# Optimization experiments

Measured on AMD Instinct MI355X. Metric: run time of the kernel, lower is better.

## Reference

```python
import jax, jax.numpy as jnp
import numpy as np

K = 20          # neighbors
EPS = 1e-5      # batch-norm eps (torch default)


def setup_inputs() -> dict:
    key = jax.random.key(0)
    k1, k2 = jax.random.split(key, 2)
    B, C, N = 16, 3, 2048
    out_dims, in_dims = 64, 2 * C
    x = jax.random.normal(k1, (B, C, N), dtype=jnp.float32)
    # Conv2d 1x1 weight, kaiming-style init as in init_layer: std = sqrt(2/(1*1*out))
    W = jax.random.normal(k2, (out_dims, in_dims), dtype=jnp.float32) * np.float32(np.sqrt(2.0 / out_dims))
    bn_weight = jnp.ones((out_dims,), dtype=jnp.float32)
    bn_bias = jnp.zeros((out_dims,), dtype=jnp.float32)
    return {"x": x, "W": W, "bn_weight": bn_weight, "bn_bias": bn_bias}


def _get_graph_feature(x, k):
    # x: (B, C, N)
    xx = jnp.sum(x * x, axis=1)                       # (B, N) squared norms
    inner = jnp.einsum('bcn,bcm->bnm', x, x)          # (B, N, N)
    pd = -xx[:, :, None] + 2.0 * inner - xx[:, None, :]  # -||xi - xj||^2
    _, idx = jax.lax.top_k(pd, k)                     # (B, N, k) nearest neighbors
    xt = jnp.transpose(x, (0, 2, 1))                  # (B, N, C)
    # gather neighbor features per batch: (N, C)[ (N, k) ] -> (N, k, C)
    neigh = jax.vmap(lambda feats, ind: feats[ind])(xt, idx)   # (B, N, k, C)
    center = jnp.broadcast_to(xt[:, :, None, :], neigh.shape)  # (B, N, k, C)
    feat = jnp.concatenate([neigh - center, center], axis=-1)  # (B, N, k, 2C)
    return jnp.transpose(feat, (0, 3, 1, 2))          # (B, 2C, N, k)


def reference(x, W, bn_weight, bn_bias):
    feat = _get_graph_feature(x, K)                   # (B, 2C, N, k)
    y = jnp.einsum('oc,bcnk->bonk', W, feat)          # 1x1 conv, no bias
    # BatchNorm2d_fw: fresh running stats + training=True -> plain batch stats
    mean = jnp.mean(y, axis=(0, 2, 3), keepdims=True)
    var = jnp.var(y, axis=(0, 2, 3), keepdims=True)   # biased variance
    yn = (y - mean) * jax.lax.rsqrt(var + EPS)
    yn = yn * bn_weight[None, :, None, None] + bn_bias[None, :, None, None]
    out = jnp.max(jax.nn.relu(yn), axis=-1)           # max over k -> (B, 64, N)
    return out
```

## Files before the change

### kernel.cpp

```cpp
#include <hip/hip_runtime.h>
#include <math.h>

#define B_   16
#define N_   2048
#define KNN  20
#define OD   64
#define M_TOT (B_ * N_ * KNN)
#define PPB  64
#define NB   64
#define CAP  96
#define BKT_BASE 468

typedef unsigned long long u64;
typedef unsigned int u32;
typedef unsigned short u16;

__global__ __launch_bounds__(512, 4) void k1_knn(const float* __restrict__ x,
                                                 float* __restrict__ stats,
                                                 int* __restrict__ idxbuf) {
    __shared__ float4 pts[N_];
    __shared__ u32    hist[NB * PPB];
    __shared__ u16    coll[PPB][CAP];
    __shared__ u32    pcnt[PPB];
    __shared__ u32    edgev[PPB];

    const int b     = blockIdx.x >> 5;
    const int chunk = blockIdx.x & 31;
    const int t     = threadIdx.x;

    const float* xb = x + b * 3 * N_;
    for (int n = t; n < N_; n += 512) {
        float x0 = xb[n], x1 = xb[N_ + n], x2 = xb[2 * N_ + n];
        float xx = x0 * x0;
        xx = fmaf(x1, x1, xx);
        xx = fmaf(x2, x2, xx);
        pts[n] = make_float4(x0, x1, x2, xx);
    }
    for (int i = t; i < NB * PPB; i += 512) hist[i] = 0;
    if (t < PPB) pcnt[t] = 0;
    __syncthreads();

    const int p  = t & 63;
    const int s  = t >> 6;
    const int il = chunk * 64 + p;
    const float4 pi = pts[il];
    const int j0 = s << 8;

    for (int jj = 0; jj < 256; jj += 8) {
        float4 q[8];
#pragma unroll
        for (int u = 0; u < 8; ++u) q[u] = pts[j0 + jj + u];
#pragma unroll
        for (int u = 0; u < 8; ++u) {
            float dot = pi.x * q[u].x;
            dot = fmaf(pi.y, q[u].y, dot);
            dot = fmaf(pi.z, q[u].z, dot);
            float pd = fmaf(2.f, dot, -pi.w) - q[u].w;
            u32 nk = __float_as_uint(pd) & 0x7FFFFFFFu;
            int bkt = (int)(nk >> 21) - BKT_BASE;
            bkt = min(max(bkt, 0), 63);
            atomicAdd(&hist[bkt * PPB + p], 1u);
        }
    }
    __syncthreads();

    if (t < PPB) {
        int cum = 0, tau = 63;
        for (int k = 0; k < NB; ++k) {
            cum += (int)hist[k * PPB + t];
            if (cum >= KNN) { tau = k; break; }
        }
        edgev[t] = (u32)(BKT_BASE + 1 + tau) << 21;
    }
    __syncthreads();

    {
        const u32 edge = edgev[p];
        for (int jj = 0; jj < 256; jj += 8) {
            float4 q[8];
#pragma unroll
            for (int u = 0; u < 8; ++u) q[u] = pts[j0 + jj + u];
#pragma unroll
            for (int u = 0; u < 8; ++u) {
                float dot = pi.x * q[u].x;
                dot = fmaf(pi.y, q[u].y, dot);
                dot = fmaf(pi.z, q[u].z, dot);
                float pd = fmaf(2.f, dot, -pi.w) - q[u].w;
                u32 nk = __float_as_uint(pd) & 0x7FFFFFFFu;
                if (nk < edge) {
                    u32 pos = atomicAdd(&pcnt[p], 1u);
                    if (pos < CAP) coll[p][pos] = (u16)(j0 + jj + u);
                }
            }
        }
    }
    __syncthreads();

    if (t < PPB) {
        const int cnt = min((int)pcnt[t], CAP);
        u64 d[KNN];
#pragma unroll
        for (int q = 0; q < KNN; ++q) d[q] = 0ull;
        for (int e = 0; e < cnt; ++e) {
            int j = coll[t][e];
            float4 pj = pts[j];
            float dot = pi.x * pj.x;
            dot = fmaf(pi.y, pj.y, dot);
            dot = fmaf(pi.z, pj.z, dot);
            float pd = fmaf(2.f, dot, -pi.w) - pj.w;
            u32 u = __float_as_uint(pd);
            u32 mono = ((int)u < 0) ? ~u : (u | 0x80000000u);
            u64 v = ((u64)mono << 32) | (u32)(~j);
            if (v > d[KNN - 1]) {
#pragma unroll
                for (int q = 0; q < KNN; ++q) {
                    u64 hi = (v > d[q]) ? v : d[q];
                    u64 lo = (v > d[q]) ? d[q] : v;
                    d[q] = hi; v = lo;
                }
            }
        }
        int ri[KNN];
#pragma unroll
        for (int r = 0; r < KNN; ++r) ri[r] = ~(u32)d[r];

        int* op = idxbuf + (b * N_ + il) * KNN;
#pragma unroll
        for (int r = 0; r < KNN; ++r) op[r] = ri[r];

        float se0 = 0.f, se1 = 0.f, se2 = 0.f;
        float see[6] = {0.f, 0.f, 0.f, 0.f, 0.f, 0.f};
#pragma unroll
        for (int r = 0; r < KNN; ++r) {
            float4 pj = pts[ri[r]];
            float e0 = pj.x - pi.x, e1 = pj.y - pi.y, e2 = pj.z - pi.z;
            se0 += e0; se1 += e1; se2 += e2;
            see[0] = fmaf(e0, e0, see[0]);
            see[1] = fmaf(e0, e1, see[1]);
            see[2] = fmaf(e0, e2, see[2]);
            see[3] = fmaf(e1, e1, see[3]);
            see[4] = fmaf(e1, e2, see[4]);
            see[5] = fmaf(e2, e2, see[5]);
        }
        float c0 = pi.x, c1 = pi.y, c2 = pi.z;
        float v[27];
        v[0] = se0; v[1] = se1; v[2] = se2;
        v[3] = 20.f * c0; v[4] = 20.f * c1; v[5] = 20.f * c2;
        v[6]  = see[0];
        v[7]  = see[1];
        v[8]  = see[2];
        v[9]  = se0 * c0;
        v[10] = se0 * c1;
        v[11] = se0 * c2;
        v[12] = see[3];
        v[13] = see[4];
        v[14] = se1 * c0;
        v[15] = se1 * c1;
        v[16] = se1 * c2;
        v[17] = see[5];
        v[18] = se2 * c0;
        v[19] = se2 * c1;
        v[20] = se2 * c2;
        v[21] = 20.f * c0 * c0;
        v[22] = 20.f * c0 * c1;
        v[23] = 20.f * c0 * c2;
        v[24] = 20.f * c1 * c1;
        v[25] = 20.f * c1 * c2;
        v[26] = 20.f * c2 * c2;

#pragma unroll
        for (int m = 0; m < 27; ++m) {
            float sm = v[m];
#pragma unroll
            for (int off = 32; off > 0; off >>= 1) sm += __shfl_xor(sm, off);
            if (t == 0) atomicAdd(stats + m, sm);
        }
    }
}

__global__ void k2_fin(const float* __restrict__ stats, const float* __restrict__ W,
                       const float* __restrict__ bnw, const float* __restrict__ bnb,
                       float* __restrict__ wp) {
    const int o = threadIdx.x;
    float m[6];
#pragma unroll
    for (int c = 0; c < 6; ++c) m[c] = stats[c];
    float S[6][6];
    int p = 6;
#pragma unroll
    for (int a = 0; a < 6; ++a)
#pragma unroll
        for (int bb = a; bb < 6; ++bb) { S[a][bb] = stats[p]; S[bb][a] = stats[p]; ++p; }
    float w[6];
#pragma unroll
    for (int c = 0; c < 6; ++c) w[c] = W[o * 6 + c];

    const float invM = 1.f / (float)M_TOT;
    float mean = 0.f;
#pragma unroll
    for (int c = 0; c < 6; ++c) mean += w[c] * m[c];
    mean *= invM;
    float ey2 = 0.f;
#pragma unroll
    for (int a = 0; a < 6; ++a)
#pragma unroll
        for (int bb = 0; bb < 6; ++bb) ey2 += w[a] * w[bb] * S[a][bb];
    ey2 *= invM;
    float var   = ey2 - mean * mean;
    float scale = bnw[o] * rsqrtf(var + 1e-5f);
    float shift = bnb[o] - mean * scale;
#pragma unroll
    for (int c = 0; c < 6; ++c) wp[o * 8 + c] = w[c] * scale;
    wp[o * 8 + 6] = shift;
    wp[o * 8 + 7] = 0.f;
}

__global__ __launch_bounds__(256, 2) void k3_out(const float* __restrict__ x,
                                                 const float* __restrict__ wp,
                                                 const int* __restrict__ idxbuf,
                                                 float* __restrict__ out) {
    __shared__ float4 pts[N_];
    __shared__ float  lwp[OD * 8];
    __shared__ int    sidx[PPB * KNN];

    const int b     = blockIdx.x >> 5;
    const int chunk = blockIdx.x & 31;
    const int t     = threadIdx.x;

    const float* xb = x + b * 3 * N_;
    for (int n = t; n < N_; n += 256)
        pts[n] = make_float4(xb[n], xb[N_ + n], xb[2 * N_ + n], 0.f);
    for (int q = t; q < OD * 8; q += 256) lwp[q] = wp[q];
    {
        const int* ib = idxbuf + (b * N_ + chunk * 64) * KNN;
        for (int i = t; i < PPB * KNN; i += 256) sidx[i] = ib[i];
    }
    __syncthreads();

    const int nl  = t & 63;
    const int sub = t >> 6;
    const int n   = chunk * 64 + nl;
    const float4 pi = pts[n];

    float e0[KNN], e1[KNN], e2[KNN];
#pragma unroll
    for (int r = 0; r < KNN; ++r) {
        int j = sidx[nl * KNN + r];
        float4 pj = pts[j];
        e0[r] = pj.x - pi.x;
        e1[r] = pj.y - pi.y;
        e2[r] = pj.z - pi.z;
    }

    float* ob = out + (size_t)b * OD * N_ + n;
    const int o0 = sub * 16;
#pragma unroll 4
    for (int o = o0; o < o0 + 16; ++o) {
        float w0 = lwp[o * 8 + 0], w1 = lwp[o * 8 + 1], w2 = lwp[o * 8 + 2];
        float w3 = lwp[o * 8 + 3], w4 = lwp[o * 8 + 4], w5 = lwp[o * 8 + 5];
        float base = lwp[o * 8 + 6];
        base = fmaf(w3, pi.x, base);
        base = fmaf(w4, pi.y, base);
        base = fmaf(w5, pi.z, base);
        float acc = 0.f;
#pragma unroll
        for (int r = 0; r < KNN; ++r) {
            float y = base;
            y = fmaf(w0, e0[r], y);
            y = fmaf(w1, e1[r], y);
            y = fmaf(w2, e2[r], y);
            acc = fmaxf(acc, y);
        }
        ob[(size_t)o * N_] = acc;
    }
}

extern "C" void kernel_launch(void* const* d_in, const int* in_sizes, int n_in,
                              void* d_out, int out_size, void* d_ws, size_t ws_size,
                              hipStream_t stream) {
    const float* x   = (const float*)d_in[0];
    const float* W   = (const float*)d_in[1];
    const float* bnw = (const float*)d_in[2];
    const float* bnb = (const float*)d_in[3];
    float* out = (float*)d_out;

    float* stats  = (float*)d_ws;
    float* wp     = (float*)((char*)d_ws + 1024);
    int*   idxbuf = (int*)((char*)d_ws + 4096);

    hipMemsetAsync(d_ws, 0, 128, stream);
    k1_knn<<<dim3(512), dim3(512), 0, stream>>>(x, stats, idxbuf);
    k2_fin<<<dim3(1), dim3(64), 0, stream>>>(stats, W, bnw, bnb, wp);
    k3_out<<<dim3(512), dim3(256), 0, stream>>>(x, wp, idxbuf, out);
}
```

Baseline: 236.0 us.

## Pack points to global once and hold candidate points in registers for KNN

Adds a pack kernel that writes float4 points with squared norms to the workspace. The KNN and output kernels then read points from global/L2 instead of staging all 2048 points per block in shared memory. In the KNN kernel each thread keeps 4 candidate points in registers and loops over query points, which are broadcast as wave-uniform loads. Blocks now cover 32 queries, doubling the grid and cutting shared memory to raise occupancy, and neighbor indices are stored as u16 to halve index traffic. The cost is one extra launch, more global and L2 reads in the gather phases, and histogram atomics that now collide across lanes on the same query's bins.

```diff
diff --git a/kernel.cpp b/kernel.cpp
--- a/kernel.cpp
+++ b/kernel.cpp
@@ -6,7 +6,7 @@
 #define KNN  20
 #define OD   64
 #define M_TOT (B_ * N_ * KNN)
-#define PPB  64
+#define PPB  32
 #define NB   64
 #define CAP  96
 #define BKT_BASE 468
@@ -15,51 +15,57 @@
 typedef unsigned int u32;
 typedef unsigned short u16;
 
-__global__ __launch_bounds__(512, 4) void k1_knn(const float* __restrict__ x,
+__global__ __launch_bounds__(256) void k0_pack(const float* __restrict__ x,
+                                               float4* __restrict__ g) {
+    int i = blockIdx.x * 256 + threadIdx.x;
+    int b = i >> 11, n = i & (N_ - 1);
+    const float* xb = x + b * 3 * N_;
+    float x0 = xb[n], x1 = xb[N_ + n], x2 = xb[2 * N_ + n];
+    float xx = x0 * x0;
+    xx = fmaf(x1, x1, xx);
+    xx = fmaf(x2, x2, xx);
+    g[i] = make_float4(x0, x1, x2, xx);
+}
+
+__global__ __launch_bounds__(512, 8) void k1_knn(const float4* __restrict__ g,
                                                  float* __restrict__ stats,
-                                                 int* __restrict__ idxbuf) {
-    __shared__ float4 pts[N_];
-    __shared__ u32    hist[NB * PPB];
-    __shared__ u16    coll[PPB][CAP];
-    __shared__ u32    pcnt[PPB];
-    __shared__ u32    edgev[PPB];
-
-    const int b     = blockIdx.x >> 5;
-    const int chunk = blockIdx.x & 31;
+                                                 u16* __restrict__ idxbuf) {
+    __shared__ u32 hist[PPB * NB];
+    __shared__ u16 coll[PPB][CAP];
+    __shared__ u32 pcnt[PPB];
+    __shared__ u32 edgev[PPB];
+
+    const int b     = blockIdx.x >> 6;
+    const int chunk = blockIdx.x & 63;
     const int t     = threadIdx.x;
-
-    const float* xb = x + b * 3 * N_;
-    for (int n = t; n < N_; n += 512) {
-        float x0 = xb[n], x1 = xb[N_ + n], x2 = xb[2 * N_ + n];
-        float xx = x0 * x0;
-        xx = fmaf(x1, x1, xx);
-        xx = fmaf(x2, x2, xx);
-        pts[n] = make_float4(x0, x1, x2, xx);
-    }
-    for (int i = t; i < NB * PPB; i += 512) hist[i] = 0;
+    const float4* gb = g + (b << 11);
+
+    for (int i = t; i < PPB * NB; i += 512) hist[i] = 0;
     if (t < PPB) pcnt[t] = 0;
     __syncthreads();
 
-    const int p  = t & 63;
-    const int s  = t >> 6;
-    const int il = chunk * 64 + p;
-    const float4 pi = pts[il];
-    const int j0 = s << 8;
-
-    for (int jj = 0; jj < 256; jj += 8) {
-        float4 q[8];
-#pragma unroll
-        for (int u = 0; u < 8; ++u) q[u] = pts[j0 + jj + u];
-#pragma unroll
-        for (int u = 0; u < 8; ++u) {
-            float dot = pi.x * q[u].x;
-            dot = fmaf(pi.y, q[u].y, dot);
-            dot = fmaf(pi.z, q[u].z, dot);
-            float pd = fmaf(2.f, dot, -pi.w) - q[u].w;
+    const int lane  = t & 63;
+    const int w     = t >> 6;
+    const int jbase = w << 8;
+
+    float4 tj[4];
+#pragma unroll
+    for (int u = 0; u < 4; ++u) tj[u] = gb[jbase + (u << 6) + lane];
+
+    const int il0 = chunk << 5;
+
+    for (int i = 0; i < PPB; ++i) {
+        int gi = __builtin_amdgcn_readfirstlane(il0 + i);
+        float4 pv = gb[gi];
+#pragma unroll
+        for (int u = 0; u < 4; ++u) {
+            float dot = pv.x * tj[u].x;
+            dot = fmaf(pv.y, tj[u].y, dot);
+            dot = fmaf(pv.z, tj[u].z, dot);
+            float pd = fmaf(2.f, dot, -pv.w) - tj[u].w;
             u32 nk = __float_as_uint(pd) & 0x7FFFFFFFu;
-            int bkt = (int)(nk >> 21) - BKT_BASE;
-            bkt = min(max(bkt, 0), 63);
-            atomicAdd(&hist[bkt * PPB + p], 1u);
+            int bkt = min(max((int)(nk >> 21) - BKT_BASE, 0), 63);
+            atomicAdd(&hist[(i << 6) + bkt], 1u);
         }
     }
     __syncthreads();
@@ -67,49 +73,48 @@
     if (t < PPB) {
         int cum = 0, tau = 63;
         for (int k = 0; k < NB; ++k) {
-            cum += (int)hist[k * PPB + t];
+            cum += (int)hist[(t << 6) + k];
             if (cum >= KNN) { tau = k; break; }
         }
         edgev[t] = (u32)(BKT_BASE + 1 + tau) << 21;
     }
     __syncthreads();
 
-    {
-        const u32 edge = edgev[p];
-        for (int jj = 0; jj < 256; jj += 8) {
-            float4 q[8];
-#pragma unroll
-            for (int u = 0; u < 8; ++u) q[u] = pts[j0 + jj + u];
-#pragma unroll
-            for (int u = 0; u < 8; ++u) {
-                float dot = pi.x * q[u].x;
-                dot = fmaf(pi.y, q[u].y, dot);
-                dot = fmaf(pi.z, q[u].z, dot);
-                float pd = fmaf(2.f, dot, -pi.w) - q[u].w;
-                u32 nk = __float_as_uint(pd) & 0x7FFFFFFFu;
-                if (nk < edge) {
-                    u32 pos = atomicAdd(&pcnt[p], 1u);
-                    if (pos < CAP) coll[p][pos] = (u16)(j0 + jj + u);
-                }
+    for (int i = 0; i < PPB; ++i) {
+        int gi = __builtin_amdgcn_readfirstlane(il0 + i);
+        float4 pv = gb[gi];
+        u32 edge = edgev[i];
+#pragma unroll
+        for (int u = 0; u < 4; ++u) {
+            float dot = pv.x * tj[u].x;
+            dot = fmaf(pv.y, tj[u].y, dot);
+            dot = fmaf(pv.z, tj[u].z, dot);
+            float pd = fmaf(2.f, dot, -pv.w) - tj[u].w;
+            u32 nk = __float_as_uint(pd) & 0x7FFFFFFFu;
+            if (nk < edge) {
+                u32 pos = atomicAdd(&pcnt[i], 1u);
+                if (pos < CAP) coll[i][pos] = (u16)(jbase + (u << 6) + lane);
             }
         }
     }
     __syncthreads();
 
     if (t < PPB) {
+        const int il = il0 + t;
+        const float4 pi = gb[il];
         const int cnt = min((int)pcnt[t], CAP);
         u64 d[KNN];
 #pragma unroll
         for (int q = 0; q < KNN; ++q) d[q] = 0ull;
         for (int e = 0; e < cnt; ++e) {
             int j = coll[t][e];
-            float4 pj = pts[j];
+            float4 pj = gb[j];
             float dot = pi.x * pj.x;
             dot = fmaf(pi.y, pj.y, dot);
             dot = fmaf(pi.z, pj.z, dot);
             float pd = fmaf(2.f, dot, -pi.w) - pj.w;
-            u32 u = __float_as_uint(pd);
-            u32 mono = ((int)u < 0) ? ~u : (u | 0x80000000u);
+            u32 uu = __float_as_uint(pd);
+            u32 mono = ((int)uu < 0) ? ~uu : (uu | 0x80000000u);
             u64 v = ((u64)mono << 32) | (u32)(~j);
             if (v > d[KNN - 1]) {
 #pragma unroll
@@ -122,17 +127,17 @@
         }
         int ri[KNN];
 #pragma unroll
-        for (int r = 0; r < KNN; ++r) ri[r] = ~(u32)d[r];
-
-        int* op = idxbuf + (b * N_ + il) * KNN;
-#pragma unroll
-        for (int r = 0; r < KNN; ++r) op[r] = ri[r];
+        for (int r = 0; r < KNN; ++r) ri[r] = (int)(~(u32)d[r]);
+
+        u16* op = idxbuf + (b * N_ + il) * KNN;
+#pragma unroll
+        for (int r = 0; r < KNN; ++r) op[r] = (u16)ri[r];
 
         float se0 = 0.f, se1 = 0.f, se2 = 0.f;
         float see[6] = {0.f, 0.f, 0.f, 0.f, 0.f, 0.f};
 #pragma unroll
         for (int r = 0; r < KNN; ++r) {
-            float4 pj = pts[ri[r]];
+            float4 pj = gb[ri[r]];
             float e0 = pj.x - pi.x, e1 = pj.y - pi.y, e2 = pj.z - pi.z;
             se0 += e0; se1 += e1; se2 += e2;
             see[0] = fmaf(e0, e0, see[0]);
@@ -172,7 +177,7 @@
         for (int m = 0; m < 27; ++m) {
             float sm = v[m];
 #pragma unroll
-            for (int off = 32; off > 0; off >>= 1) sm += __shfl_xor(sm, off);
+            for (int off = 16; off > 0; off >>= 1) sm += __shfl_xor(sm, off);
             if (t == 0) atomicAdd(stats + m, sm);
         }
     }
@@ -215,47 +220,44 @@
     wp[o * 8 + 7] = 0.f;
 }
 
-__global__ __launch_bounds__(256, 2) void k3_out(const float* __restrict__ x,
-                                                 const float* __restrict__ wp,
-                                                 const int* __restrict__ idxbuf,
-                                                 float* __restrict__ out) {
-    __shared__ float4 pts[N_];
-    __shared__ float  lwp[OD * 8];
-    __shared__ int    sidx[PPB * KNN];
-
-    const int b     = blockIdx.x >> 5;
-    const int chunk = blockIdx.x & 31;
+__global__ __launch_bounds__(256) void k3_out(const float4* __restrict__ g,
+                                              const float* __restrict__ wp,
+                                              const u16* __restrict__ idxbuf,
+                                              float* __restrict__ out) {
+    __shared__ float lwp[OD * 8];
+    __shared__ u16   sidx[PPB * KNN];
+
+    const int b     = blockIdx.x >> 6;
+    const int chunk = blockIdx.x & 63;
     const int t     = threadIdx.x;
-
-    const float* xb = x + b * 3 * N_;
-    for (int n = t; n < N_; n += 256)
-        pts[n] = make_float4(xb[n], xb[N_ + n], xb[2 * N_ + n], 0.f);
+    const float4* gb = g + (b << 11);
+
     for (int q = t; q < OD * 8; q += 256) lwp[q] = wp[q];
     {
-        const int* ib = idxbuf + (b * N_ + chunk * 64) * KNN;
+        const u16* ib = idxbuf + (b * N_ + (chunk << 5)) * KNN;
         for (int i = t; i < PPB * KNN; i += 256) sidx[i] = ib[i];
     }
     __syncthreads();
 
-    const int nl  = t & 63;
-    const int sub = t >> 6;
-    const int n   = chunk * 64 + nl;
-    const float4 pi = pts[n];
+    const int nl  = t & 31;
+    const int sub = t >> 5;
+    const int n   = (chunk << 5) + nl;
+    const float4 pi = gb[n];
 
     float e0[KNN], e1[KNN], e2[KNN];
 #pragma unroll
     for (int r = 0; r < KNN; ++r) {
         int j = sidx[nl * KNN + r];
-        float4 pj = pts[j];
+        float4 pj = gb[j];
         e0[r] = pj.x - pi.x;
         e1[r] = pj.y - pi.y;
         e2[r] = pj.z - pi.z;
     }
 
     float* ob = out + (size_t)b * OD * N_ + n;
-    const int o0 = sub * 16;
-#pragma unroll 4
-    for (int o = o0; o < o0 + 16; ++o) {
+    const int o0 = sub * 8;
+#pragma unroll
+    for (int o = o0; o < o0 + 8; ++o) {
         float w0 = lwp[o * 8 + 0], w1 = lwp[o * 8 + 1], w2 = lwp[o * 8 + 2];
         float w3 = lwp[o * 8 + 3], w4 = lwp[o * 8 + 4], w5 = lwp[o * 8 + 5];
         float base = lwp[o * 8 + 6];
@@ -284,12 +286,14 @@
     const float* bnb = (const float*)d_in[3];
     float* out = (float*)d_out;
 
-    float* stats  = (float*)d_ws;
-    float* wp     = (float*)((char*)d_ws + 1024);
-    int*   idxbuf = (int*)((char*)d_ws + 4096);
+    float*  stats  = (float*)d_ws;
+    float*  wp     = (float*)((char*)d_ws + 1024);
+    float4* pts_g  = (float4*)((char*)d_ws + 4096);
+    u16*    idxbuf = (u16*)((char*)d_ws + 4096 + 524288);
 
     hipMemsetAsync(d_ws, 0, 128, stream);
-    k1_knn<<<dim3(512), dim3(512), 0, stream>>>(x, stats, idxbuf);
+    k0_pack<<<dim3(128), dim3(256), 0, stream>>>(x, pts_g);
+    k1_knn<<<dim3(1024), dim3(512), 0, stream>>>(pts_g, stats, idxbuf);
     k2_fin<<<dim3(1), dim3(64), 0, stream>>>(stats, W, bnw, bnb, wp);
-    k3_out<<<dim3(512), dim3(256), 0, stream>>>(x, wp, idxbuf, out);
-}
+    k3_out<<<dim3(1024), dim3(256), 0, stream>>>(pts_g, wp, idxbuf, out);
+}
```

Measured after the change: 363.6 us. 1.54x slower.

## Pre-pack points globally, read from L1/scalar loads, and emit edge vectors for output kernel

Applied to the files above, without the earlier changes.

Adds a pack kernel that writes (x,y,z,|x|^2) float4 points to workspace once. The KNN kernel now reads points directly from global memory with wave-uniform indices instead of staging all 2048 points into LDS, and it writes per-neighbor edge vectors in a coalesced layout. The output kernel loads those precomputed edge vectors instead of re-gathering by index, and register-blocks 8 output channels per pass. This trades LDS staging and redundant gathers for more global traffic and an extra launch.

```diff
diff --git a/kernel.cpp b/kernel.cpp
--- a/kernel.cpp
+++ b/kernel.cpp
@@ -15,51 +15,54 @@
 typedef unsigned int u32;
 typedef unsigned short u16;
 
-__global__ __launch_bounds__(512, 4) void k1_knn(const float* __restrict__ x,
+__global__ __launch_bounds__(256) void k0_pack(const float* __restrict__ x,
+                                               float4* __restrict__ g) {
+    int i = blockIdx.x * 256 + threadIdx.x;
+    int b = i >> 11, n = i & (N_ - 1);
+    const float* xb = x + b * 3 * N_;
+    float x0 = xb[n], x1 = xb[N_ + n], x2 = xb[2 * N_ + n];
+    float xx = x0 * x0;
+    xx = fmaf(x1, x1, xx);
+    xx = fmaf(x2, x2, xx);
+    g[i] = make_float4(x0, x1, x2, xx);
+}
+
+__global__ __launch_bounds__(512, 4) void k1_knn(const float4* __restrict__ g,
                                                  float* __restrict__ stats,
-                                                 int* __restrict__ idxbuf) {
-    __shared__ float4 pts[N_];
-    __shared__ u32    hist[NB * PPB];
-    __shared__ u16    coll[PPB][CAP];
-    __shared__ u32    pcnt[PPB];
-    __shared__ u32    edgev[PPB];
+                                                 float4* __restrict__ evec) {
+    __shared__ u32 hist[NB * PPB];
+    __shared__ u16 coll[PPB][CAP];
+    __shared__ u32 pcnt[PPB];
+    __shared__ u32 edgev[PPB];
 
     const int b     = blockIdx.x >> 5;
     const int chunk = blockIdx.x & 31;
     const int t     = threadIdx.x;
-
-    const float* xb = x + b * 3 * N_;
-    for (int n = t; n < N_; n += 512) {
-        float x0 = xb[n], x1 = xb[N_ + n], x2 = xb[2 * N_ + n];
-        float xx = x0 * x0;
-        xx = fmaf(x1, x1, xx);
-        xx = fmaf(x2, x2, xx);
-        pts[n] = make_float4(x0, x1, x2, xx);
-    }
+    const float4* gb = g + (b << 11);
+
+    const int lane = t & 63;
+    const int il   = (chunk << 6) + lane;
+    const float4 pi = gb[il];
+
     for (int i = t; i < NB * PPB; i += 512) hist[i] = 0;
     if (t < PPB) pcnt[t] = 0;
     __syncthreads();
 
-    const int p  = t & 63;
-    const int s  = t >> 6;
-    const int il = chunk * 64 + p;
-    const float4 pi = pts[il];
-    const int j0 = s << 8;
-
-    for (int jj = 0; jj < 256; jj += 8) {
-        float4 q[8];
-#pragma unroll
-        for (int u = 0; u < 8; ++u) q[u] = pts[j0 + jj + u];
-#pragma unroll
-        for (int u = 0; u < 8; ++u) {
+    const int jw = __builtin_amdgcn_readfirstlane((t >> 6) << 8);
+
+    for (int jj = 0; jj < 256; jj += 4) {
+        float4 q[4];
+#pragma unroll
+        for (int u = 0; u < 4; ++u) q[u] = gb[jw + jj + u];
+#pragma unroll
+        for (int u = 0; u < 4; ++u) {
             float dot = pi.x * q[u].x;
             dot = fmaf(pi.y, q[u].y, dot);
             dot = fmaf(pi.z, q[u].z, dot);
             float pd = fmaf(2.f, dot, -pi.w) - q[u].w;
             u32 nk = __float_as_uint(pd) & 0x7FFFFFFFu;
-            int bkt = (int)(nk >> 21) - BKT_BASE;
-            bkt = min(max(bkt, 0), 63);
-            atomicAdd(&hist[bkt * PPB + p], 1u);
+            int bkt = min(max((int)(nk >> 21) - BKT_BASE, 0), 63);
+            atomicAdd(&hist[(bkt << 6) + lane], 1u);
         }
     }
     __syncthreads();
@@ -67,7 +70,7 @@
     if (t < PPB) {
         int cum = 0, tau = 63;
         for (int k = 0; k < NB; ++k) {
-            cum += (int)hist[k * PPB + t];
+            cum += (int)hist[(k << 6) + t];
             if (cum >= KNN) { tau = k; break; }
         }
         edgev[t] = (u32)(BKT_BASE + 1 + tau) << 21;
@@ -75,21 +78,21 @@
     __syncthreads();
 
     {
-        const u32 edge = edgev[p];
-        for (int jj = 0; jj < 256; jj += 8) {
-            float4 q[8];
-#pragma unroll
-            for (int u = 0; u < 8; ++u) q[u] = pts[j0 + jj + u];
-#pragma unroll
-            for (int u = 0; u < 8; ++u) {
+        const u32 edge = edgev[lane];
+        for (int jj = 0; jj < 256; jj += 4) {
+            float4 q[4];
+#pragma unroll
+            for (int u = 0; u < 4; ++u) q[u] = gb[jw + jj + u];
+#pragma unroll
+            for (int u = 0; u < 4; ++u) {
                 float dot = pi.x * q[u].x;
                 dot = fmaf(pi.y, q[u].y, dot);
                 dot = fmaf(pi.z, q[u].z, dot);
                 float pd = fmaf(2.f, dot, -pi.w) - q[u].w;
                 u32 nk = __float_as_uint(pd) & 0x7FFFFFFFu;
                 if (nk < edge) {
-                    u32 pos = atomicAdd(&pcnt[p], 1u);
-                    if (pos < CAP) coll[p][pos] = (u16)(j0 + jj + u);
+                    u32 pos = atomicAdd(&pcnt[lane], 1u);
+                    if (pos < CAP) coll[lane][pos] = (u16)(jw + jj + u);
                 }
             }
         }
@@ -103,13 +106,13 @@
         for (int q = 0; q < KNN; ++q) d[q] = 0ull;
         for (int e = 0; e < cnt; ++e) {
             int j = coll[t][e];
-            float4 pj = pts[j];
+            float4 pj = gb[j];
             float dot = pi.x * pj.x;
             dot = fmaf(pi.y, pj.y, dot);
             dot = fmaf(pi.z, pj.z, dot);
             float pd = fmaf(2.f, dot, -pi.w) - pj.w;
-            u32 u = __float_as_uint(pd);
-            u32 mono = ((int)u < 0) ? ~u : (u | 0x80000000u);
+            u32 uu = __float_as_uint(pd);
+            u32 mono = ((int)uu < 0) ? ~uu : (uu | 0x80000000u);
             u64 v = ((u64)mono << 32) | (u32)(~j);
             if (v > d[KNN - 1]) {
 #pragma unroll
@@ -120,20 +123,16 @@
                 }
             }
         }
-        int ri[KNN];
-#pragma unroll
-        for (int r = 0; r < KNN; ++r) ri[r] = ~(u32)d[r];
-
-        int* op = idxbuf + (b * N_ + il) * KNN;
-#pragma unroll
-        for (int r = 0; r < KNN; ++r) op[r] = ri[r];
-
+
+        float4* ep = evec + ((b * KNN) << 11) + il;
         float se0 = 0.f, se1 = 0.f, se2 = 0.f;
         float see[6] = {0.f, 0.f, 0.f, 0.f, 0.f, 0.f};
 #pragma unroll
         for (int r = 0; r < KNN; ++r) {
-            float4 pj = pts[ri[r]];
+            int j = (int)(~(u32)d[r]);
+            float4 pj = gb[j];
             float e0 = pj.x - pi.x, e1 = pj.y - pi.y, e2 = pj.z - pi.z;
+            ep[r << 11] = make_float4(e0, e1, e2, 0.f);
             se0 += e0; se1 += e1; se2 += e2;
             see[0] = fmaf(e0, e0, see[0]);
             see[1] = fmaf(e0, e1, see[1]);
@@ -215,63 +214,60 @@
     wp[o * 8 + 7] = 0.f;
 }
 
-__global__ __launch_bounds__(256, 2) void k3_out(const float* __restrict__ x,
-                                                 const float* __restrict__ wp,
-                                                 const int* __restrict__ idxbuf,
-                                                 float* __restrict__ out) {
-    __shared__ float4 pts[N_];
+__global__ __launch_bounds__(256) void k3_out(const float4* __restrict__ g,
+                                              const float* __restrict__ wp,
+                                              const float4* __restrict__ evec,
+                                              float* __restrict__ out) {
+    __shared__ float4 sev[PPB * KNN];
     __shared__ float  lwp[OD * 8];
-    __shared__ int    sidx[PPB * KNN];
 
     const int b     = blockIdx.x >> 5;
     const int chunk = blockIdx.x & 31;
     const int t     = threadIdx.x;
-
-    const float* xb = x + b * 3 * N_;
-    for (int n = t; n < N_; n += 256)
-        pts[n] = make_float4(xb[n], xb[N_ + n], xb[2 * N_ + n], 0.f);
+    const int n0    = chunk << 6;
+
     for (int q = t; q < OD * 8; q += 256) lwp[q] = wp[q];
-    {
-        const int* ib = idxbuf + (b * N_ + chunk * 64) * KNN;
-        for (int i = t; i < PPB * KNN; i += 256) sidx[i] = ib[i];
+    for (int i = t; i < PPB * KNN; i += 256) {
+        int r = i >> 6, nn = i & 63;
+        sev[i] = evec[((b * KNN + r) << 11) + n0 + nn];
     }
     __syncthreads();
 
     const int nl  = t & 63;
     const int sub = t >> 6;
-    const int n   = chunk * 64 + nl;
-    const float4 pi = pts[n];
-
-    float e0[KNN], e1[KNN], e2[KNN];
-#pragma unroll
-    for (int r = 0; r < KNN; ++r) {
-        int j = sidx[nl * KNN + r];
-        float4 pj = pts[j];
-        e0[r] = pj.x - pi.x;
-        e1[r] = pj.y - pi.y;
-        e2[r] = pj.z - pi.z;
-    }
-
+    const int n   = n0 + nl;
+    const float4 pi = g[(b << 11) + n];
     float* ob = out + (size_t)b * OD * N_ + n;
-    const int o0 = sub * 16;
-#pragma unroll 4
-    for (int o = o0; o < o0 + 16; ++o) {
-        float w0 = lwp[o * 8 + 0], w1 = lwp[o * 8 + 1], w2 = lwp[o * 8 + 2];
-        float w3 = lwp[o * 8 + 3], w4 = lwp[o * 8 + 4], w5 = lwp[o * 8 + 5];
-        float base = lwp[o * 8 + 6];
-        base = fmaf(w3, pi.x, base);
-        base = fmaf(w4, pi.y, base);
-        base = fmaf(w5, pi.z, base);
-        float acc = 0.f;
+
+#pragma unroll
+    for (int cb = 0; cb < 2; ++cb) {
+        const int o0 = sub * 16 + cb * 8;
+        float w0[8], w1[8], w2[8], bs[8], acc[8];
+#pragma unroll
+        for (int c = 0; c < 8; ++c) {
+            const float* wo = &lwp[(o0 + c) * 8];
+            w0[c] = wo[0]; w1[c] = wo[1]; w2[c] = wo[2];
+            float base = wo[6];
+            base = fmaf(wo[3], pi.x, base);
+            base = fmaf(wo[4], pi.y, base);
+            base = fmaf(wo[5], pi.z, base);
+            bs[c] = base;
+            acc[c] = 0.f;
+        }
 #pragma unroll
         for (int r = 0; r < KNN; ++r) {
-            float y = base;
-            y = fmaf(w0, e0[r], y);
-            y = fmaf(w1, e1[r], y);
-            y = fmaf(w2, e2[r], y);
-            acc = fmaxf(acc, y);
-        }
-        ob[(size_t)o * N_] = acc;
+            float4 e = sev[(r << 6) + nl];
+#pragma unroll
+            for (int c = 0; c < 8; ++c) {
+                float y = bs[c];
+                y = fmaf(w0[c], e.x, y);
+                y = fmaf(w1[c], e.y, y);
+                y = fmaf(w2[c], e.z, y);
+                acc[c] = fmaxf(acc[c], y);
+            }
+        }
+#pragma unroll
+        for (int c = 0; c < 8; ++c) ob[(size_t)(o0 + c) << 11] = acc[c];
     }
 }
 
@@ -284,12 +280,14 @@
     const float* bnb = (const float*)d_in[3];
     float* out = (float*)d_out;
 
-    float* stats  = (float*)d_ws;
-    float* wp     = (float*)((char*)d_ws + 1024);
-    int*   idxbuf = (int*)((char*)d_ws + 4096);
+    float*  stats = (float*)d_ws;
+    float*  wp    = (float*)((char*)d_ws + 1024);
+    float4* pts_g = (float4*)((char*)d_ws + 4096);
+    float4* evec  = (float4*)((char*)d_ws + 4096 + 524288);
 
     hipMemsetAsync(d_ws, 0, 128, stream);
-    k1_knn<<<dim3(512), dim3(512), 0, stream>>>(x, stats, idxbuf);
+    k0_pack<<<dim3(128), dim3(256), 0, stream>>>(x, pts_g);
+    k1_knn<<<dim3(512), dim3(512), 0, stream>>>(pts_g, stats, evec);
     k2_fin<<<dim3(1), dim3(64), 0, stream>>>(stats, W, bnw, bnb, wp);
-    k3_out<<<dim3(512), dim3(256), 0, stream>>>(x, wp, idxbuf, out);
-}
+    k3_out<<<dim3(512), dim3(256), 0, stream>>>(pts_g, wp, evec, out);
+}
```

Result: slower. 250.9 us (+6.3%).
